# Kernel tuning notes

Measured on AMD Instinct MI355X. Metric: run time of the kernel, lower is better.

## Reference

```python
import jax, jax.numpy as jnp
import numpy as np

B, N = 4, 2048
NFEAT, NHID, NHEADS, NCLASS = 512, 64, 4, 64
ALPHA = 0.2  # leaky relu negative slope
AVG_DEG = 32.0


def setup_inputs() -> dict:
    key = jax.random.key(0)
    ks = jax.random.split(key, 6)
    x = jax.random.normal(ks[0], (B, N, NFEAT), jnp.float32)
    # sparse binary adjacency (~AVG_DEG neighbors/node) + self-loops so rowsums > 0
    adj = jax.random.bernoulli(ks[1], AVG_DEG / N, (N, N)).astype(jnp.float32)
    adj = jnp.maximum(adj, jnp.eye(N, dtype=jnp.float32))
    W1 = jax.random.normal(ks[2], (NHEADS, NFEAT, NHID), jnp.float32) * (1.0 / np.sqrt(NFEAT))
    a1 = jax.random.normal(ks[3], (NHEADS, 2 * NHID), jnp.float32) * 0.1
    W2 = jax.random.normal(ks[4], (NHEADS * NHID, NCLASS), jnp.float32) * (1.0 / np.sqrt(NHEADS * NHID))
    a2 = jax.random.normal(ks[5], (2 * NCLASS,), jnp.float32) * 0.1
    return {"x": x, "adj": adj, "W1": W1, "a1": a1, "W2": W2, "a2": a2}


def reference(x, adj, W1, a1, W2, a2):
    # Dropout layers run in eval mode (identity) for a deterministic reference.
    # --- multi-head SpGraphAttentionLayer, concat=True ---
    h = jnp.einsum('bnf,hfd->bhnd', x, W1)                      # [B,H,N,D]
    s_src = jnp.einsum('bhnd,hd->bhn', h, a1[:, :NHID])
    s_dst = jnp.einsum('bhnd,hd->bhn', h, a1[:, NHID:])
    # pyGAT sparse layer: edge_e = exp(-leakyrelu(a . [h_i || h_j])), masked by adj
    e = jnp.exp(-jax.nn.leaky_relu(s_src[..., :, None] + s_dst[..., None, :], ALPHA)) * adj  # [B,H,N,N]
    num = jnp.einsum('bhnm,bhmd->bhnd', e, h)
    den = jnp.sum(e, axis=-1, keepdims=True)
    h1 = jax.nn.elu(num / den)                                  # concat=True -> elu inside layer
    h1 = jnp.transpose(h1, (0, 2, 1, 3)).reshape(B, N, NHEADS * NHID)  # head concat
    # --- output SpGraphAttentionLayer, concat=False ---
    g = h1 @ W2                                                 # [B,N,C]
    t_src = g @ a2[:NCLASS]
    t_dst = g @ a2[NCLASS:]
    e2 = jnp.exp(-jax.nn.leaky_relu(t_src[..., :, None] + t_dst[..., None, :], ALPHA)) * adj  # [B,N,N]
    out = jnp.einsum('bnm,bmd->bnd', e2, g) / jnp.sum(e2, axis=-1, keepdims=True)
    return jax.nn.elu(out)                                      # outer F.elu in SpGAT.forward
```

## Files before the change

### kernel.cpp

```cpp
#include <hip/hip_runtime.h>
#include <hip/hip_bf16.h>

constexpr int B_ = 4, N_ = 2048, NFEAT = 512, NHID = 64, NHEADS = 4, NCLASS = 64;
constexpr int MAXDEG = 128;
#define LRELU_ALPHA 0.2f

typedef __attribute__((ext_vector_type(8))) short short8;
typedef __attribute__((ext_vector_type(4))) float f32x4;

__device__ __forceinline__ unsigned short f2bf_rne(float f) {
  unsigned int u = __float_as_uint(f);
  unsigned int r = (u + 0x7FFFu + ((u >> 16) & 1u)) >> 16;
  return (unsigned short)r;
}
__device__ __forceinline__ float bf2f(unsigned short h) {
  return __uint_as_float(((unsigned int)h) << 16);
}

__global__ __launch_bounds__(256) void build_adj_kernel(
    const float* __restrict__ adj, int* __restrict__ nbr, int* __restrict__ deg) {
  int n = blockIdx.x;
  int tid = threadIdx.x;
  __shared__ int cnt;
  if (tid == 0) cnt = 0;
  __syncthreads();
  for (int m = tid; m < N_; m += 256) {
    bool nz = adj[(size_t)n * N_ + m] != 0.0f;
    unsigned long long mask = __ballot(nz);
    int lane = tid & 63;
    int num = __popcll(mask);
    if (num) {
      int base = 0;
      if (lane == 0) base = atomicAdd(&cnt, num);
      base = __shfl(base, 0);
      if (nz) {
        int pos = base + __popcll(mask & ((1ull << lane) - 1ull));
        if (pos < MAXDEG) nbr[n * MAXDEG + pos] = m;
      }
    }
  }
  __syncthreads();
  if (tid == 0) deg[n] = cnt < MAXDEG ? cnt : MAXDEG;
}

__global__ __launch_bounds__(256) void prep_x_kernel(
    const float* __restrict__ x, unsigned short* __restrict__ xhi,
    unsigned short* __restrict__ xlo) {
  size_t idx = ((size_t)blockIdx.x * 256 + threadIdx.x) * 8;
  float4 v0 = *(const float4*)&x[idx];
  float4 v1 = *(const float4*)&x[idx + 4];
  float v[8] = {v0.x, v0.y, v0.z, v0.w, v1.x, v1.y, v1.z, v1.w};
  short8 sh, sl;
#pragma unroll
  for (int j = 0; j < 8; ++j) {
    unsigned short hi = f2bf_rne(v[j]);
    sh[j] = (short)hi;
    sl[j] = (short)f2bf_rne(v[j] - bf2f(hi));
  }
  *(short8*)&xhi[idx] = sh;
  *(short8*)&xlo[idx] = sl;
}

__global__ __launch_bounds__(256) void prep_w_kernel(
    const float* __restrict__ W1, unsigned short* __restrict__ wth,
    unsigned short* __restrict__ wtl) {
  __shared__ float ts[64][65];
  int h = blockIdx.y, k0 = blockIdx.x * 64;
  int tid = threadIdx.x;
  int kr = tid >> 2, nc = (tid & 3) * 16;
  const float* src = W1 + ((size_t)h * NFEAT + k0 + kr) * 64 + nc;
#pragma unroll
  for (int j = 0; j < 4; ++j)
    *(float4*)&ts[kr][nc + 4 * j] = *(const float4*)(src + 4 * j);
  __syncthreads();
  int n = tid >> 2, kc = (tid & 3) * 16;
  short8 h0, h1v, l0, l1v;
#pragma unroll
  for (int j = 0; j < 8; ++j) {
    float a = ts[kc + j][n];
    float b = ts[kc + 8 + j][n];
    unsigned short ah = f2bf_rne(a), bh = f2bf_rne(b);
    h0[j] = (short)ah; h1v[j] = (short)bh;
    l0[j] = (short)f2bf_rne(a - bf2f(ah));
    l1v[j] = (short)f2bf_rne(b - bf2f(bh));
  }
  size_t o = ((size_t)h * 64 + n) * NFEAT + k0 + kc;
  *(short8*)&wth[o]     = h0;
  *(short8*)&wth[o + 8] = h1v;
  *(short8*)&wtl[o]     = l0;
  *(short8*)&wtl[o + 8] = l1v;
}

__global__ __launch_bounds__(256) void gemm1_mfma_kernel(
    const unsigned short* __restrict__ xhi, const unsigned short* __restrict__ xlo,
    const unsigned short* __restrict__ wth, const unsigned short* __restrict__ wtl,
    float* __restrict__ Y) {
  __shared__ unsigned short xsh[64][72], xsl[64][72], wsh[64][72], wsl[64][72];
  int tid = threadIdx.x;
  int w = tid >> 6, l = tid & 63;
  int row0 = blockIdx.x * 64;
  int head = blockIdx.y;
  const unsigned short* xh = xhi + (size_t)row0 * NFEAT;
  const unsigned short* xl = xlo + (size_t)row0 * NFEAT;
  const unsigned short* wh = wth + (size_t)head * 64 * NFEAT;
  const unsigned short* wl = wtl + (size_t)head * 64 * NFEAT;

  int sr = tid >> 2;
  int sc = (tid & 3) * 16;

  f32x4 acc[4];
#pragma unroll
  for (int nt = 0; nt < 4; ++nt) acc[nt] = (f32x4){0.f, 0.f, 0.f, 0.f};

  for (int k0 = 0; k0 < NFEAT; k0 += 64) {
    {
      const unsigned short* s0 = xh + (size_t)sr * NFEAT + k0 + sc;
      const unsigned short* s1 = xl + (size_t)sr * NFEAT + k0 + sc;
      const unsigned short* s2 = wh + (size_t)sr * NFEAT + k0 + sc;
      const unsigned short* s3 = wl + (size_t)sr * NFEAT + k0 + sc;
      *(short8*)&xsh[sr][sc]     = *(const short8*)s0;
      *(short8*)&xsh[sr][sc + 8] = *(const short8*)(s0 + 8);
      *(short8*)&xsl[sr][sc]     = *(const short8*)s1;
      *(short8*)&xsl[sr][sc + 8] = *(const short8*)(s1 + 8);
      *(short8*)&wsh[sr][sc]     = *(const short8*)s2;
      *(short8*)&wsh[sr][sc + 8] = *(const short8*)(s2 + 8);
      *(short8*)&wsl[sr][sc]     = *(const short8*)s3;
      *(short8*)&wsl[sr][sc + 8] = *(const short8*)(s3 + 8);
    }
    __syncthreads();
#pragma unroll
    for (int ks = 0; ks < 2; ++ks) {
      int ko = ks * 32 + (l >> 4) * 8;
      int ar = 16 * w + (l & 15);
      short8 ah = *(const short8*)&xsh[ar][ko];
      short8 al = *(const short8*)&xsl[ar][ko];
#pragma unroll
      for (int nt = 0; nt < 4; ++nt) {
        int br = 16 * nt + (l & 15);
        short8 bh = *(const short8*)&wsh[br][ko];
        short8 bl = *(const short8*)&wsl[br][ko];
        acc[nt] = __builtin_amdgcn_mfma_f32_16x16x32_bf16(ah, bh, acc[nt], 0, 0, 0);
        acc[nt] = __builtin_amdgcn_mfma_f32_16x16x32_bf16(ah, bl, acc[nt], 0, 0, 0);
        acc[nt] = __builtin_amdgcn_mfma_f32_16x16x32_bf16(al, bh, acc[nt], 0, 0, 0);
      }
    }
    __syncthreads();
  }

  int b = row0 >> 11;
  int nbase = row0 & (N_ - 1);
#pragma unroll
  for (int nt = 0; nt < 4; ++nt) {
#pragma unroll
    for (int j = 0; j < 4; ++j) {
      int r = 16 * w + (l >> 4) * 4 + j;
      Y[(((size_t)(b * NHEADS + head)) * N_ + nbase + r) * 64 + 16 * nt + (l & 15)] =
          acc[nt][j];
    }
  }
}

template <int K>
__global__ __launch_bounds__(256) void gemm_kernel(
    const float* __restrict__ X, const float* __restrict__ W, float* __restrict__ Y) {
  __shared__ float xs_t[64][68];
  __shared__ float ws[64][68];
  int tid = threadIdx.x;
  int tc4 = (tid & 15) * 4;
  int tr4 = (tid >> 4) * 4;
  int row0 = blockIdx.x * 64;
  const float* Xb = X + (size_t)row0 * K;
  const float* Wb = W;
  int sr = tid >> 2;
  int sc = (tid & 3) * 16;
  float4 acc[4];
#pragma unroll
  for (int i = 0; i < 4; ++i) acc[i] = make_float4(0.f, 0.f, 0.f, 0.f);

  for (int fc = 0; fc < K; fc += 64) {
    {
      const float* src = Xb + (size_t)sr * K + fc + sc;
      float v[16];
      *(float4*)&v[0]  = ((const float4*)src)[0];
      *(float4*)&v[4]  = ((const float4*)src)[1];
      *(float4*)&v[8]  = ((const float4*)src)[2];
      *(float4*)&v[12] = ((const float4*)src)[3];
#pragma unroll
      for (int j = 0; j < 16; ++j) xs_t[sc + j][sr] = v[j];
    }
    {
      const float* src = Wb + (size_t)(fc + sr) * 64 + sc;
      *(float4*)&ws[sr][sc]      = ((const float4*)src)[0];
      *(float4*)&ws[sr][sc + 4]  = ((const float4*)src)[1];
      *(float4*)&ws[sr][sc + 8]  = ((const float4*)src)[2];
      *(float4*)&ws[sr][sc + 12] = ((const float4*)src)[3];
    }
    __syncthreads();
#pragma unroll 8
    for (int f = 0; f < 64; ++f) {
      float4 xv = *(const float4*)&xs_t[f][tr4];
      float4 wv = *(const float4*)&ws[f][tc4];
      acc[0].x = fmaf(xv.x, wv.x, acc[0].x);
      acc[0].y = fmaf(xv.x, wv.y, acc[0].y);
      acc[0].z = fmaf(xv.x, wv.z, acc[0].z);
      acc[0].w = fmaf(xv.x, wv.w, acc[0].w);
      acc[1].x = fmaf(xv.y, wv.x, acc[1].x);
      acc[1].y = fmaf(xv.y, wv.y, acc[1].y);
      acc[1].z = fmaf(xv.y, wv.z, acc[1].z);
      acc[1].w = fmaf(xv.y, wv.w, acc[1].w);
      acc[2].x = fmaf(xv.z, wv.x, acc[2].x);
      acc[2].y = fmaf(xv.z, wv.y, acc[2].y);
      acc[2].z = fmaf(xv.z, wv.z, acc[2].z);
      acc[2].w = fmaf(xv.z, wv.w, acc[2].w);
      acc[3].x = fmaf(xv.w, wv.x, acc[3].x);
      acc[3].y = fmaf(xv.w, wv.y, acc[3].y);
      acc[3].z = fmaf(xv.w, wv.z, acc[3].z);
      acc[3].w = fmaf(xv.w, wv.w, acc[3].w);
    }
    __syncthreads();
  }
#pragma unroll
  for (int i = 0; i < 4; ++i) {
    int gr = row0 + tr4 + i;
    *(float4*)&Y[(size_t)gr * 64 + tc4] = acc[i];
  }
}

template <int NH>
__global__ __launch_bounds__(256) void rowdot_kernel(
    const float* __restrict__ Hm, const float* __restrict__ a,
    float* __restrict__ ssrc, float* __restrict__ sdst) {
  int w = threadIdx.x >> 6, lane = threadIdx.x & 63;
  int gr = blockIdx.x * 4 + w;
  int hh = (NH > 1) ? ((gr >> 11) & (NH - 1)) : 0;
  float v = Hm[(size_t)gr * 64 + lane];
  float s1 = v * a[hh * 128 + lane];
  float s2 = v * a[hh * 128 + 64 + lane];
#pragma unroll
  for (int off = 32; off; off >>= 1) {
    s1 += __shfl_xor(s1, off);
    s2 += __shfl_xor(s2, off);
  }
  if (lane == 0) { ssrc[gr] = s1; sdst[gr] = s2; }
}

__device__ __forceinline__ float sparse_agg(
    const float* __restrict__ plane, const float* __restrict__ sdb,
    const int* __restrict__ nb, int dg, float ss, int lane) {
  float acc0 = 0.f, acc1 = 0.f, den0 = 0.f, den1 = 0.f;
  int k = 0;
  for (; k + 8 <= dg; k += 8) {
    int m[8];
    float sv[8], hv[8];
#pragma unroll
    for (int j = 0; j < 8; ++j) m[j] = nb[k + j];
#pragma unroll
    for (int j = 0; j < 8; ++j) sv[j] = sdb[m[j]];
#pragma unroll
    for (int j = 0; j < 8; ++j) hv[j] = plane[(size_t)m[j] * 64 + lane];
#pragma unroll
    for (int j = 0; j < 8; ++j) {
      float s = ss + sv[j];
      float lr = s > 0.f ? s : LRELU_ALPHA * s;
      float ev = __expf(-lr);
      if (j & 1) { den1 += ev; acc1 = fmaf(ev, hv[j], acc1); }
      else       { den0 += ev; acc0 = fmaf(ev, hv[j], acc0); }
    }
  }
  for (; k < dg; ++k) {
    int m = nb[k];
    float s = ss + sdb[m];
    float lr = s > 0.f ? s : LRELU_ALPHA * s;
    float ev = __expf(-lr);
    den0 += ev;
    acc0 = fmaf(ev, plane[(size_t)m * 64 + lane], acc0);
  }
  return (acc0 + acc1) / (den0 + den1);
}

__global__ __launch_bounds__(256) void attn1_kernel(
    const float* __restrict__ Hm, const float* __restrict__ ssrc,
    const float* __restrict__ sdst, const int* __restrict__ nbr,
    const int* __restrict__ deg, float* __restrict__ h1) {
  int w = threadIdx.x >> 6, lane = threadIdx.x & 63;
  int gr = blockIdx.x * 4 + w;
  int n = gr & (N_ - 1);
  int bh = gr >> 11;
  float o = sparse_agg(Hm + (size_t)bh * N_ * 64, sdst + (size_t)bh * N_,
                       nbr + n * MAXDEG, deg[n], ssrc[gr], lane);
  o = o > 0.f ? o : expm1f(o);
  int b = bh >> 2, hh = bh & 3;
  h1[((size_t)b * N_ + n) * (NHEADS * NHID) + hh * 64 + lane] = o;
}

__global__ __launch_bounds__(256) void attn2_kernel(
    const float* __restrict__ G, const float* __restrict__ tsrc,
    const float* __restrict__ tdst, const int* __restrict__ nbr,
    const int* __restrict__ deg, float* __restrict__ out) {
  int w = threadIdx.x >> 6, lane = threadIdx.x & 63;
  int gr = blockIdx.x * 4 + w;
  int n = gr & (N_ - 1);
  int b = gr >> 11;
  float o = sparse_agg(G + (size_t)b * N_ * 64, tdst + (size_t)b * N_,
                       nbr + n * MAXDEG, deg[n], tsrc[gr], lane);
  out[(size_t)gr * 64 + lane] = o > 0.f ? o : expm1f(o);
}

extern "C" void kernel_launch(void* const* d_in, const int* in_sizes, int n_in,
                              void* d_out, int out_size, void* d_ws, size_t ws_size,
                              hipStream_t stream) {
  const float* x   = (const float*)d_in[0];
  const float* adj = (const float*)d_in[1];
  const float* W1  = (const float*)d_in[2];
  const float* a1  = (const float*)d_in[3];
  const float* W2  = (const float*)d_in[4];
  const float* a2  = (const float*)d_in[5];
  float* out = (float*)d_out;

  char* ws = (char*)d_ws;
  float* h    = (float*)ws; ws += (size_t)B_ * NHEADS * N_ * 64 * 4;
  float* h1   = (float*)ws; ws += (size_t)B_ * N_ * 256 * 4;
  float* g    = (float*)ws; ws += (size_t)B_ * N_ * 64 * 4;
  float* ssrc = (float*)ws; ws += (size_t)B_ * NHEADS * N_ * 4;
  float* sdst = (float*)ws; ws += (size_t)B_ * NHEADS * N_ * 4;
  float* tsrc = (float*)ws; ws += (size_t)B_ * N_ * 4;
  float* tdst = (float*)ws; ws += (size_t)B_ * N_ * 4;
  int*   nbr  = (int*)ws;   ws += (size_t)N_ * MAXDEG * 4;
  int*   deg  = (int*)ws;   ws += (size_t)N_ * 4;
  ws = (char*)(((size_t)ws + 255) & ~(size_t)255);
  unsigned short* xhi = (unsigned short*)ws; ws += (size_t)B_ * N_ * NFEAT * 2;
  unsigned short* xlo = (unsigned short*)ws; ws += (size_t)B_ * N_ * NFEAT * 2;
  unsigned short* wth = (unsigned short*)ws; ws += (size_t)NHEADS * 64 * NFEAT * 2;
  unsigned short* wtl = (unsigned short*)ws; ws += (size_t)NHEADS * 64 * NFEAT * 2;

  build_adj_kernel<<<N_, 256, 0, stream>>>(adj, nbr, deg);
  prep_x_kernel<<<(B_ * N_ * NFEAT) / (256 * 8), 256, 0, stream>>>(x, xhi, xlo);
  prep_w_kernel<<<dim3(NFEAT / 64, NHEADS), 256, 0, stream>>>(W1, wth, wtl);
  gemm1_mfma_kernel<<<dim3(B_ * N_ / 64, NHEADS), 256, 0, stream>>>(xhi, xlo, wth, wtl, h);
  rowdot_kernel<NHEADS><<<B_ * NHEADS * N_ / 4, 256, 0, stream>>>(h, a1, ssrc, sdst);
  attn1_kernel<<<B_ * NHEADS * N_ / 4, 256, 0, stream>>>(h, ssrc, sdst, nbr, deg, h1);
  gemm_kernel<NHEADS * NHID><<<B_ * N_ / 64, 256, 0, stream>>>(h1, W2, g);
  rowdot_kernel<1><<<B_ * N_ / 4, 256, 0, stream>>>(g, a2, tsrc, tdst);
  attn2_kernel<<<B_ * N_ / 4, 256, 0, stream>>>(g, tsrc, tdst, nbr, deg, out);
}
```

Baseline: 167.0 us.

## Fuse attention-score rowdots into MFMA GEMMs and run GEMM2 on split-bf16 MFMA

```diff
diff --git a/kernel.cpp b/kernel.cpp
--- a/kernel.cpp
+++ b/kernel.cpp
@@ -61,14 +61,15 @@
   *(short8*)&xlo[idx] = sl;
 }
 
+template <int KK>
 __global__ __launch_bounds__(256) void prep_w_kernel(
-    const float* __restrict__ W1, unsigned short* __restrict__ wth,
+    const float* __restrict__ W, unsigned short* __restrict__ wth,
     unsigned short* __restrict__ wtl) {
   __shared__ float ts[64][65];
   int h = blockIdx.y, k0 = blockIdx.x * 64;
   int tid = threadIdx.x;
   int kr = tid >> 2, nc = (tid & 3) * 16;
-  const float* src = W1 + ((size_t)h * NFEAT + k0 + kr) * 64 + nc;
+  const float* src = W + ((size_t)h * KK + k0 + kr) * 64 + nc;
 #pragma unroll
   for (int j = 0; j < 4; ++j)
     *(float4*)&ts[kr][nc + 4 * j] = *(const float4*)(src + 4 * j);
@@ -84,26 +85,29 @@
     l0[j] = (short)f2bf_rne(a - bf2f(ah));
     l1v[j] = (short)f2bf_rne(b - bf2f(bh));
   }
-  size_t o = ((size_t)h * 64 + n) * NFEAT + k0 + kc;
+  size_t o = ((size_t)h * 64 + n) * KK + k0 + kc;
   *(short8*)&wth[o]     = h0;
   *(short8*)&wth[o + 8] = h1v;
   *(short8*)&wtl[o]     = l0;
   *(short8*)&wtl[o + 8] = l1v;
 }
 
-__global__ __launch_bounds__(256) void gemm1_mfma_kernel(
-    const unsigned short* __restrict__ xhi, const unsigned short* __restrict__ xlo,
-    const unsigned short* __restrict__ wth, const unsigned short* __restrict__ wtl,
-    float* __restrict__ Y) {
+template <int K, int MODE>
+__global__ __launch_bounds__(256) void gemm_mfma_kernel(
+    const unsigned short* __restrict__ Xh, const unsigned short* __restrict__ Xl,
+    const unsigned short* __restrict__ Wth, const unsigned short* __restrict__ Wtl,
+    const float* __restrict__ avec, float* __restrict__ Y,
+    float* __restrict__ so_src, float* __restrict__ so_dst) {
   __shared__ unsigned short xsh[64][72], xsl[64][72], wsh[64][72], wsl[64][72];
   int tid = threadIdx.x;
   int w = tid >> 6, l = tid & 63;
   int row0 = blockIdx.x * 64;
   int head = blockIdx.y;
-  const unsigned short* xh = xhi + (size_t)row0 * NFEAT;
-  const unsigned short* xl = xlo + (size_t)row0 * NFEAT;
-  const unsigned short* wh = wth + (size_t)head * 64 * NFEAT;
-  const unsigned short* wl = wtl + (size_t)head * 64 * NFEAT;
+  const unsigned short* xh = Xh + (size_t)row0 * K;
+  const unsigned short* xl = Xl + (size_t)row0 * K;
+  const unsigned short* wh = Wth + (size_t)head * 64 * K;
+  const unsigned short* wl = Wtl + (size_t)head * 64 * K;
+  const float* av = avec + head * 128;
 
   int sr = tid >> 2;
   int sc = (tid & 3) * 16;
@@ -112,12 +116,12 @@
 #pragma unroll
   for (int nt = 0; nt < 4; ++nt) acc[nt] = (f32x4){0.f, 0.f, 0.f, 0.f};
 
-  for (int k0 = 0; k0 < NFEAT; k0 += 64) {
+  for (int k0 = 0; k0 < K; k0 += 64) {
     {
-      const unsigned short* s0 = xh + (size_t)sr * NFEAT + k0 + sc;
-      const unsigned short* s1 = xl + (size_t)sr * NFEAT + k0 + sc;
-      const unsigned short* s2 = wh + (size_t)sr * NFEAT + k0 + sc;
-      const unsigned short* s3 = wl + (size_t)sr * NFEAT + k0 + sc;
+      const unsigned short* s0 = xh + (size_t)sr * K + k0 + sc;
+      const unsigned short* s1 = xl + (size_t)sr * K + k0 + sc;
+      const unsigned short* s2 = wh + (size_t)sr * K + k0 + sc;
+      const unsigned short* s3 = wl + (size_t)sr * K + k0 + sc;
       *(short8*)&xsh[sr][sc]     = *(const short8*)s0;
       *(short8*)&xsh[sr][sc + 8] = *(const short8*)(s0 + 8);
       *(short8*)&xsl[sr][sc]     = *(const short8*)s1;
@@ -147,103 +151,60 @@
     __syncthreads();
   }
 
-  int b = row0 >> 11;
-  int nbase = row0 & (N_ - 1);
+  int col = (l & 15);
 #pragma unroll
   for (int nt = 0; nt < 4; ++nt) {
 #pragma unroll
     for (int j = 0; j < 4; ++j) {
       int r = 16 * w + (l >> 4) * 4 + j;
-      Y[(((size_t)(b * NHEADS + head)) * N_ + nbase + r) * 64 + 16 * nt + (l & 15)] =
-          acc[nt][j];
-    }
-  }
-}
-
-template <int K>
-__global__ __launch_bounds__(256) void gemm_kernel(
-    const float* __restrict__ X, const float* __restrict__ W, float* __restrict__ Y) {
-  __shared__ float xs_t[64][68];
-  __shared__ float ws[64][68];
-  int tid = threadIdx.x;
-  int tc4 = (tid & 15) * 4;
-  int tr4 = (tid >> 4) * 4;
-  int row0 = blockIdx.x * 64;
-  const float* Xb = X + (size_t)row0 * K;
-  const float* Wb = W;
-  int sr = tid >> 2;
-  int sc = (tid & 3) * 16;
-  float4 acc[4];
-#pragma unroll
-  for (int i = 0; i < 4; ++i) acc[i] = make_float4(0.f, 0.f, 0.f, 0.f);
-
-  for (int fc = 0; fc < K; fc += 64) {
-    {
-      const float* src = Xb + (size_t)sr * K + fc + sc;
-      float v[16];
-      *(float4*)&v[0]  = ((const float4*)src)[0];
-      *(float4*)&v[4]  = ((const float4*)src)[1];
-      *(float4*)&v[8]  = ((const float4*)src)[2];
-      *(float4*)&v[12] = ((const float4*)src)[3];
-#pragma unroll
-      for (int j = 0; j < 16; ++j) xs_t[sc + j][sr] = v[j];
-    }
-    {
-      const float* src = Wb + (size_t)(fc + sr) * 64 + sc;
-      *(float4*)&ws[sr][sc]      = ((const float4*)src)[0];
-      *(float4*)&ws[sr][sc + 4]  = ((const float4*)src)[1];
-      *(float4*)&ws[sr][sc + 8]  = ((const float4*)src)[2];
-      *(float4*)&ws[sr][sc + 12] = ((const float4*)src)[3];
-    }
-    __syncthreads();
-#pragma unroll 8
-    for (int f = 0; f < 64; ++f) {
-      float4 xv = *(const float4*)&xs_t[f][tr4];
-      float4 wv = *(const float4*)&ws[f][tc4];
-      acc[0].x = fmaf(xv.x, wv.x, acc[0].x);
-      acc[0].y = fmaf(xv.x, wv.y, acc[0].y);
-      acc[0].z = fmaf(xv.x, wv.z, acc[0].z);
-      acc[0].w = fmaf(xv.x, wv.w, acc[0].w);
-      acc[1].x = fmaf(xv.y, wv.x, acc[1].x);
-      acc[1].y = fmaf(xv.y, wv.y, acc[1].y);
-      acc[1].z = fmaf(xv.y, wv.z, acc[1].z);
-      acc[1].w = fmaf(xv.y, wv.w, acc[1].w);
-      acc[2].x = fmaf(xv.z, wv.x, acc[2].x);
-      acc[2].y = fmaf(xv.z, wv.y, acc[2].y);
-      acc[2].z = fmaf(xv.z, wv.z, acc[2].z);
-      acc[2].w = fmaf(xv.z, wv.w, acc[2].w);
-      acc[3].x = fmaf(xv.w, wv.x, acc[3].x);
-      acc[3].y = fmaf(xv.w, wv.y, acc[3].y);
-      acc[3].z = fmaf(xv.w, wv.z, acc[3].z);
-      acc[3].w = fmaf(xv.w, wv.w, acc[3].w);
-    }
-    __syncthreads();
-  }
-#pragma unroll
-  for (int i = 0; i < 4; ++i) {
-    int gr = row0 + tr4 + i;
-    *(float4*)&Y[(size_t)gr * 64 + tc4] = acc[i];
-  }
-}
-
-template <int NH>
-__global__ __launch_bounds__(256) void rowdot_kernel(
-    const float* __restrict__ Hm, const float* __restrict__ a,
-    float* __restrict__ ssrc, float* __restrict__ sdst) {
-  int w = threadIdx.x >> 6, lane = threadIdx.x & 63;
-  int gr = blockIdx.x * 4 + w;
-  int hh = (NH > 1) ? ((gr >> 11) & (NH - 1)) : 0;
-  float v = Hm[(size_t)gr * 64 + lane];
-  float s1 = v * a[hh * 128 + lane];
-  float s2 = v * a[hh * 128 + 64 + lane];
-#pragma unroll
-  for (int off = 32; off; off >>= 1) {
-    s1 += __shfl_xor(s1, off);
-    s2 += __shfl_xor(s2, off);
-  }
-  if (lane == 0) { ssrc[gr] = s1; sdst[gr] = s2; }
-}
-
+      size_t gr = row0 + r;
+      if (MODE == 0)
+        Y[gr * (NHEADS * 64) + head * 64 + 16 * nt + col] = acc[nt][j];
+      else
+        Y[gr * 64 + 16 * nt + col] = acc[nt][j];
+    }
+  }
+  float aS[4], aD[4];
+#pragma unroll
+  for (int nt = 0; nt < 4; ++nt) {
+    aS[nt] = av[16 * nt + col];
+    aD[nt] = av[64 + 16 * nt + col];
+  }
+  float s1[4] = {0.f, 0.f, 0.f, 0.f}, s2[4] = {0.f, 0.f, 0.f, 0.f};
+#pragma unroll
+  for (int nt = 0; nt < 4; ++nt)
+#pragma unroll
+    for (int j = 0; j < 4; ++j) {
+      s1[j] = fmaf(acc[nt][j], aS[nt], s1[j]);
+      s2[j] = fmaf(acc[nt][j], aD[nt], s2[j]);
+    }
+#pragma unroll
+  for (int off = 1; off < 16; off <<= 1) {
+#pragma unroll
+    for (int j = 0; j < 4; ++j) {
+      s1[j] += __shfl_xor(s1[j], off);
+      s2[j] += __shfl_xor(s2[j], off);
+    }
+  }
+  if (col == 0) {
+#pragma unroll
+    for (int j = 0; j < 4; ++j) {
+      int r = 16 * w + (l >> 4) * 4 + j;
+      int gr = row0 + r;
+      size_t si;
+      if (MODE == 0) {
+        int b = gr >> 11, n = gr & (N_ - 1);
+        si = (size_t)(b * NHEADS + head) * N_ + n;
+      } else {
+        si = gr;
+      }
+      so_src[si] = s1[j];
+      so_dst[si] = s2[j];
+    }
+  }
+}
+
+template <int RS>
 __device__ __forceinline__ float sparse_agg(
     const float* __restrict__ plane, const float* __restrict__ sdb,
     const int* __restrict__ nb, int dg, float ss, int lane) {
@@ -257,7 +218,7 @@
 #pragma unroll
     for (int j = 0; j < 8; ++j) sv[j] = sdb[m[j]];
 #pragma unroll
-    for (int j = 0; j < 8; ++j) hv[j] = plane[(size_t)m[j] * 64 + lane];
+    for (int j = 0; j < 8; ++j) hv[j] = plane[(size_t)m[j] * RS + lane];
 #pragma unroll
     for (int j = 0; j < 8; ++j) {
       float s = ss + sv[j];
@@ -273,7 +234,7 @@
     float lr = s > 0.f ? s : LRELU_ALPHA * s;
     float ev = __expf(-lr);
     den0 += ev;
-    acc0 = fmaf(ev, plane[(size_t)m * 64 + lane], acc0);
+    acc0 = fmaf(ev, plane[(size_t)m * RS + lane], acc0);
   }
   return (acc0 + acc1) / (den0 + den1);
 }
@@ -281,16 +242,26 @@
 __global__ __launch_bounds__(256) void attn1_kernel(
     const float* __restrict__ Hm, const float* __restrict__ ssrc,
     const float* __restrict__ sdst, const int* __restrict__ nbr,
-    const int* __restrict__ deg, float* __restrict__ h1) {
-  int w = threadIdx.x >> 6, lane = threadIdx.x & 63;
-  int gr = blockIdx.x * 4 + w;
-  int n = gr & (N_ - 1);
-  int bh = gr >> 11;
-  float o = sparse_agg(Hm + (size_t)bh * N_ * 64, sdst + (size_t)bh * N_,
-                       nbr + n * MAXDEG, deg[n], ssrc[gr], lane);
+    const int* __restrict__ deg, unsigned short* __restrict__ h1h,
+    unsigned short* __restrict__ h1l) {
+  int bn = blockIdx.x;
+  int n = bn & (N_ - 1), b = bn >> 11;
+  int w = threadIdx.x >> 6;
+  int lane = threadIdx.x & 63;
+  __shared__ int lds_nbr[MAXDEG];
+  int dg = deg[n];
+  for (int k = threadIdx.x; k < dg; k += 256) lds_nbr[k] = nbr[n * MAXDEG + k];
+  __syncthreads();
+  int bh = b * NHEADS + w;
+  float ss = ssrc[(size_t)bh * N_ + n];
+  const float* sdb = sdst + (size_t)bh * N_;
+  const float* plane = Hm + (size_t)b * N_ * (NHEADS * 64) + w * 64;
+  float o = sparse_agg<NHEADS * 64>(plane, sdb, lds_nbr, dg, ss, lane);
   o = o > 0.f ? o : expm1f(o);
-  int b = bh >> 2, hh = bh & 3;
-  h1[((size_t)b * N_ + n) * (NHEADS * NHID) + hh * 64 + lane] = o;
+  unsigned short hi = f2bf_rne(o);
+  size_t oi = (size_t)bn * (NHEADS * NHID) + w * 64 + lane;
+  h1h[oi] = hi;
+  h1l[oi] = f2bf_rne(o - bf2f(hi));
 }
 
 __global__ __launch_bounds__(256) void attn2_kernel(
@@ -301,8 +272,8 @@
   int gr = blockIdx.x * 4 + w;
   int n = gr & (N_ - 1);
   int b = gr >> 11;
-  float o = sparse_agg(G + (size_t)b * N_ * 64, tdst + (size_t)b * N_,
-                       nbr + n * MAXDEG, deg[n], tsrc[gr], lane);
+  float o = sparse_agg<64>(G + (size_t)b * N_ * 64, tdst + (size_t)b * N_,
+                           nbr + n * MAXDEG, deg[n], tsrc[gr], lane);
   out[(size_t)gr * 64 + lane] = o > 0.f ? o : expm1f(o);
 }
 
@@ -318,8 +289,7 @@
   float* out = (float*)d_out;
 
   char* ws = (char*)d_ws;
-  float* h    = (float*)ws; ws += (size_t)B_ * NHEADS * N_ * 64 * 4;
-  float* h1   = (float*)ws; ws += (size_t)B_ * N_ * 256 * 4;
+  float* h    = (float*)ws; ws += (size_t)B_ * N_ * 256 * 4;
   float* g    = (float*)ws; ws += (size_t)B_ * N_ * 64 * 4;
   float* ssrc = (float*)ws; ws += (size_t)B_ * NHEADS * N_ * 4;
   float* sdst = (float*)ws; ws += (size_t)B_ * NHEADS * N_ * 4;
@@ -328,18 +298,23 @@
   int*   nbr  = (int*)ws;   ws += (size_t)N_ * MAXDEG * 4;
   int*   deg  = (int*)ws;   ws += (size_t)N_ * 4;
   ws = (char*)(((size_t)ws + 255) & ~(size_t)255);
-  unsigned short* xhi = (unsigned short*)ws; ws += (size_t)B_ * N_ * NFEAT * 2;
-  unsigned short* xlo = (unsigned short*)ws; ws += (size_t)B_ * N_ * NFEAT * 2;
-  unsigned short* wth = (unsigned short*)ws; ws += (size_t)NHEADS * 64 * NFEAT * 2;
-  unsigned short* wtl = (unsigned short*)ws; ws += (size_t)NHEADS * 64 * NFEAT * 2;
+  unsigned short* xhi  = (unsigned short*)ws; ws += (size_t)B_ * N_ * NFEAT * 2;
+  unsigned short* xlo  = (unsigned short*)ws; ws += (size_t)B_ * N_ * NFEAT * 2;
+  unsigned short* wt1h = (unsigned short*)ws; ws += (size_t)NHEADS * 64 * NFEAT * 2;
+  unsigned short* wt1l = (unsigned short*)ws; ws += (size_t)NHEADS * 64 * NFEAT * 2;
+  unsigned short* wt2h = (unsigned short*)ws; ws += (size_t)64 * 256 * 2;
+  unsigned short* wt2l = (unsigned short*)ws; ws += (size_t)64 * 256 * 2;
+  unsigned short* h1h  = (unsigned short*)ws; ws += (size_t)B_ * N_ * 256 * 2;
+  unsigned short* h1l  = (unsigned short*)ws; ws += (size_t)B_ * N_ * 256 * 2;
 
   build_adj_kernel<<<N_, 256, 0, stream>>>(adj, nbr, deg);
   prep_x_kernel<<<(B_ * N_ * NFEAT) / (256 * 8), 256, 0, stream>>>(x, xhi, xlo);
-  prep_w_kernel<<<dim3(NFEAT / 64, NHEADS), 256, 0, stream>>>(W1, wth, wtl);
-  gemm1_mfma_kernel<<<dim3(B_ * N_ / 64, NHEADS), 256, 0, stream>>>(xhi, xlo, wth, wtl, h);
-  rowdot_kernel<NHEADS><<<B_ * NHEADS * N_ / 4, 256, 0, stream>>>(h, a1, ssrc, sdst);
-  attn1_kernel<<<B_ * NHEADS * N_ / 4, 256, 0, stream>>>(h, ssrc, sdst, nbr, deg, h1);
-  gemm_kernel<NHEADS * NHID><<<B_ * N_ / 64, 256, 0, stream>>>(h1, W2, g);
-  rowdot_kernel<1><<<B_ * N_ / 4, 256, 0, stream>>>(g, a2, tsrc, tdst);
+  prep_w_kernel<NFEAT><<<dim3(NFEAT / 64, NHEADS), 256, 0, stream>>>(W1, wt1h, wt1l);
+  prep_w_kernel<256><<<dim3(256 / 64, 1), 256, 0, stream>>>(W2, wt2h, wt2l);
+  gemm_mfma_kernel<NFEAT, 0><<<dim3(B_ * N_ / 64, NHEADS), 256, 0, stream>>>(
+      xhi, xlo, wt1h, wt1l, a1, h, ssrc, sdst);
+  attn1_kernel<<<B_ * N_, 256, 0, stream>>>(h, ssrc, sdst, nbr, deg, h1h, h1l);
+  gemm_mfma_kernel<256, 1><<<dim3(B_ * N_ / 64, 1), 256, 0, stream>>>(
+      h1h, h1l, wt2h, wt2l, a2, g, tsrc, tdst);
   attn2_kernel<<<B_ * N_ / 4, 256, 0, stream>>>(g, tsrc, tdst, nbr, deg, out);
 }
```

Result: faster. 149.2 us (-10.7%).
